# Kernel optimization log

Hardware: AMD Instinct MI355X
Metric: run time of the kernel (lower is better)

Reference implementation:

```python
import jax, jax.numpy as jnp
import numpy as np

N = 50000      # nodes
E = 1_600_000  # edges per metapath graph
M = 3          # meta-path patterns
D = 128        # feature dim (in_size == out_size, GraphConv has no weight)
H = 128        # semantic-attention hidden size


def setup_inputs() -> dict:
    key = jax.random.key(0)
    k1, k2, k3, k4 = jax.random.split(key, 4)
    h = jax.random.normal(k1, (N, D), dtype=jnp.float32)
    # edges[m, 0] = src node ids, edges[m, 1] = dst node ids for metapath m
    edges = jax.random.randint(k2, (M, 2, E), 0, N, dtype=jnp.int32)
    W1 = jax.random.normal(k3, (D, H), dtype=jnp.float32) * 0.05
    b1 = jnp.zeros((H,), dtype=jnp.float32)
    W2 = jax.random.normal(k4, (H, 1), dtype=jnp.float32) * 0.05
    return {"h": h, "edges": edges, "W1": W1, "b1": b1, "W2": W2}


def _graph_conv_both(h, src, dst, n):
    """DGL GraphConv(norm='both', weight=None, bias=None):
    out = D_in^{-1/2} * A @ (D_out^{-1/2} * h), zero degrees clamped to 1."""
    ones = jnp.ones_like(src, dtype=h.dtype)
    out_deg = jax.ops.segment_sum(ones, src, num_segments=n)
    in_deg = jax.ops.segment_sum(ones, dst, num_segments=n)
    norm_src = jax.lax.rsqrt(jnp.maximum(out_deg, 1.0))
    norm_dst = jax.lax.rsqrt(jnp.maximum(in_deg, 1.0))
    msg = (h * norm_src[:, None])[src]                  # [E, D] gather
    agg = jax.ops.segment_sum(msg, dst, num_segments=n)  # [N, D] scatter-add
    return agg * norm_dst[:, None]


def reference(h, edges, W1, b1, W2):
    n = h.shape[0]
    m = edges.shape[0]
    # One normalized sparse aggregation per meta-path (fixed small M).
    z = jnp.stack(
        [_graph_conv_both(h, edges[i, 0], edges[i, 1], n) for i in range(m)],
        axis=1,
    )  # [N, M, D]
    # Semantic attention: project -> tanh -> score, mean over nodes, softmax over M.
    w = jnp.mean(jnp.tanh(z @ W1 + b1) @ W2, axis=0)  # [M, 1]
    beta = jax.nn.softmax(w, axis=0)                  # [M, 1]
    return jnp.sum(beta[None, :, :] * z, axis=1)      # [N, D]
```

## Files before the change

kernel.cpp:

```cpp
#include <hip/hip_runtime.h>
#include <cstdint>
#include <cstddef>

typedef unsigned int  uint;
typedef unsigned short ushort;
typedef short bf16x8 __attribute__((ext_vector_type(8)));
typedef float f32x4  __attribute__((ext_vector_type(4)));

#define N_NODES 50000
#define N_EDGES 1600000
#define N_META  3
#define DIM     128

#define BKT       128
#define NBKT      391
#define BIN_CHUNK 4096
#define NCHUNK    391
#define CSR_CAP   5504
#define OCH       128
#define EPC       (N_EDGES / OCH)
#define OWORDS    12500
#define PREP_A    (N_META * OCH)
#define W1C_B     4

#define AT_TILE   64
#define AT_NBLK   782

__device__ __forceinline__ uint bf16rne(float f) {
    const uint u = __float_as_uint(f);
    return (u + 0x7FFFu + ((u >> 16) & 1u)) >> 16;
}
__device__ __forceinline__ float bflo(uint p) { return __uint_as_float(p << 16); }
__device__ __forceinline__ float bfhi(uint p) { return __uint_as_float(p & 0xFFFF0000u); }
__device__ __forceinline__ float fast_tanh(float x) {
    const float e = __expf(2.0f * x);
    return 1.0f - 2.0f / (e + 1.0f);
}

__global__ __launch_bounds__(256) void prep_kernel(
        const int* __restrict__ edges, const float* __restrict__ W1,
        int* __restrict__ bucket_cnt, uint* __restrict__ partials,
        ushort* __restrict__ W1T) {
    __shared__ __align__(16) uint sh[OWORDS];
    __shared__ uint bh[NBKT];
    const int blk = blockIdx.x;
    if (blk < PREP_A) {
        const int m = blk >> 7, c = blk & 127;
        uint4* sh4 = reinterpret_cast<uint4*>(sh);
        for (int j = threadIdx.x; j < OWORDS / 4; j += 256)
            sh4[j] = make_uint4(0u, 0u, 0u, 0u);
        for (int j = threadIdx.x; j < NBKT; j += 256) bh[j] = 0;
        __syncthreads();
        const int* src = edges + (size_t)(2 * m) * N_EDGES;
        const int* dst = edges + (size_t)(2 * m + 1) * N_EDGES;
        const int beg = c * EPC;
        for (int i = beg + 4 * threadIdx.x; i + 4 <= beg + EPC; i += 1024) {
            const uint4 s4 = *reinterpret_cast<const uint4*>(src + i);
            const uint4 d4 = *reinterpret_cast<const uint4*>(dst + i);
            atomicAdd(&sh[s4.x >> 2], 1u << (8 * (s4.x & 3)));
            atomicAdd(&sh[s4.y >> 2], 1u << (8 * (s4.y & 3)));
            atomicAdd(&sh[s4.z >> 2], 1u << (8 * (s4.z & 3)));
            atomicAdd(&sh[s4.w >> 2], 1u << (8 * (s4.w & 3)));
            atomicAdd(&bh[d4.x >> 7], 1u);
            atomicAdd(&bh[d4.y >> 7], 1u);
            atomicAdd(&bh[d4.z >> 7], 1u);
            atomicAdd(&bh[d4.w >> 7], 1u);
        }
        __syncthreads();
        uint4* outp4 = reinterpret_cast<uint4*>(
            partials + (size_t)(m * OCH + c) * OWORDS);
        for (int j = threadIdx.x; j < OWORDS / 4; j += 256) outp4[j] = sh4[j];
        for (int j = threadIdx.x; j < NBKT; j += 256)
            if (bh[j]) atomicAdd(&bucket_cnt[m * NBKT + j], (int)bh[j]);
    } else {
        const int base = (blk - PREP_A) * (DIM * DIM / W1C_B);
        for (int o = base + threadIdx.x; o < base + DIM * DIM / W1C_B; o += 256) {
            const int j = o >> 7, k = o & 127;
            W1T[o] = (ushort)bf16rne(W1[k * DIM + j]);
        }
    }
}

__global__ __launch_bounds__(512) void scan_nsrc_kernel(
        const int* __restrict__ bucket_cnt, int* __restrict__ bucket_off,
        int* __restrict__ bucket_cur, int* __restrict__ row_off,
        const uint* __restrict__ partials, float* __restrict__ nsrc) {
    const int blk = blockIdx.x;
    if (blk < N_META) {
        __shared__ int sc[512];
        const int m = blk, t = threadIdx.x;
        const int v = (t < NBKT) ? bucket_cnt[m * NBKT + t] : 0;
        sc[t] = v;
        __syncthreads();
        for (int off = 1; off < 512; off <<= 1) {
            const int tt = (t >= off) ? sc[t - off] : 0;
            __syncthreads();
            sc[t] += tt;
            __syncthreads();
        }
        const int excl = sc[t] - v;
        if (t < NBKT) {
            bucket_off[m * (NBKT + 1) + t] = excl;
            bucket_cur[m * NBKT + t] = excl;
        }
        if (t == 0) {
            bucket_off[m * (NBKT + 1) + NBKT] = N_EDGES;
            row_off[m * (N_NODES + 1) + N_NODES] = N_EDGES;
        }
    } else {
        const int i = (blk - N_META) * 512 + threadIdx.x;
        if (i < N_META * N_NODES) {
            const int m = i / N_NODES, node = i - m * N_NODES;
            const int q = node >> 2, s8 = 8 * (node & 3);
            int s = 0;
#pragma unroll 8
            for (int c = 0; c < OCH; ++c)
                s += (partials[(size_t)(m * OCH + c) * OWORDS + q] >> s8) & 0xFF;
            nsrc[i] = rsqrtf(fmaxf((float)s, 1.0f));
        }
    }
}

__global__ __launch_bounds__(256) void scale_kernel(
        const float* __restrict__ h, const float* __restrict__ nsrc,
        ushort* __restrict__ hbm) {
    const int i = blockIdx.x * 256 + threadIdx.x;
    const int node = i >> 5;
    const float4 v = reinterpret_cast<const float4*>(h)[i];
    uint2* o = reinterpret_cast<uint2*>(hbm);
#pragma unroll
    for (int m = 0; m < N_META; ++m) {
        const float n = nsrc[m * N_NODES + node];
        uint2 p;
        p.x = bf16rne(v.x * n) | (bf16rne(v.y * n) << 16);
        p.y = bf16rne(v.z * n) | (bf16rne(v.w * n) << 16);
        o[(size_t)m * (N_NODES * DIM / 4) + i] = p;
    }
}

__global__ __launch_bounds__(256) void bin_kernel(
        const int* __restrict__ edges, int* __restrict__ bucket_cur,
        uint* __restrict__ pairs) {
    const int m = blockIdx.y;
    __shared__ int hist[NBKT];
    __shared__ int cur[NBKT];
    for (int j = threadIdx.x; j < NBKT; j += 256) hist[j] = 0;
    __syncthreads();
    const int* src = edges + (size_t)(2 * m) * N_EDGES;
    const int* dst = edges + (size_t)(2 * m + 1) * N_EDGES;
    const int beg = blockIdx.x * BIN_CHUNK;
    const int end = min(beg + BIN_CHUNK, N_EDGES);
    for (int i = beg + 4 * threadIdx.x; i + 4 <= end; i += 1024) {
        const uint4 d4 = *reinterpret_cast<const uint4*>(dst + i);
        atomicAdd(&hist[d4.x >> 7], 1);
        atomicAdd(&hist[d4.y >> 7], 1);
        atomicAdd(&hist[d4.z >> 7], 1);
        atomicAdd(&hist[d4.w >> 7], 1);
    }
    __syncthreads();
    for (int j = threadIdx.x; j < NBKT; j += 256) {
        const int n = hist[j];
        cur[j] = n ? atomicAdd(&bucket_cur[m * NBKT + j], n) : 0;
    }
    __syncthreads();
    uint* pm = pairs + (size_t)m * N_EDGES;
    for (int i = beg + 4 * threadIdx.x; i + 4 <= end; i += 1024) {
        const uint4 s4 = *reinterpret_cast<const uint4*>(src + i);
        const uint4 d4 = *reinterpret_cast<const uint4*>(dst + i);
        int p0 = atomicAdd(&cur[d4.x >> 7], 1);
        pm[p0] = (d4.x << 16) | s4.x;
        int p1 = atomicAdd(&cur[d4.y >> 7], 1);
        pm[p1] = (d4.y << 16) | s4.y;
        int p2 = atomicAdd(&cur[d4.z >> 7], 1);
        pm[p2] = (d4.z << 16) | s4.z;
        int p3 = atomicAdd(&cur[d4.w >> 7], 1);
        pm[p3] = (d4.w << 16) | s4.w;
    }
}

__global__ __launch_bounds__(128) void csr_kernel(
        const uint* __restrict__ pairs, const int* __restrict__ bucket_off,
        int* __restrict__ row_off, ushort* __restrict__ csr) {
    const int b = blockIdx.x, m = blockIdx.y;
    const int node_base = b * BKT;
    const int nb = min(BKT, N_NODES - node_base);
    __shared__ uint stage[CSR_CAP];
    __shared__ int hist[BKT];
    __shared__ int sc[BKT];
    __shared__ int cur[BKT];
    hist[threadIdx.x] = 0;
    __syncthreads();
    const int beg = bucket_off[m * (NBKT + 1) + b];
    const int end = bucket_off[m * (NBKT + 1) + b + 1];
    const int cnt = end - beg;
    const uint* pm = pairs + (size_t)m * N_EDGES + beg;
    for (int i = threadIdx.x; i < cnt; i += 128) {
        const uint p = pm[i];
        if (i < CSR_CAP) stage[i] = p;
        atomicAdd(&hist[(int)(p >> 16) - node_base], 1);
    }
    __syncthreads();
    const int v = hist[threadIdx.x];
    sc[threadIdx.x] = v;
    __syncthreads();
    for (int off = 1; off < BKT; off <<= 1) {
        const int t = (threadIdx.x >= off) ? sc[threadIdx.x - off] : 0;
        __syncthreads();
        sc[threadIdx.x] += t;
        __syncthreads();
    }
    const int excl = sc[threadIdx.x] - v;
    cur[threadIdx.x] = beg + excl;
    if (threadIdx.x < nb)
        row_off[m * (N_NODES + 1) + node_base + threadIdx.x] = beg + excl;
    __syncthreads();
    ushort* cm = csr + (size_t)m * N_EDGES;
    for (int i = threadIdx.x; i < cnt; i += 128) {
        const uint p = (i < CSR_CAP) ? stage[i] : pm[i];
        const int dl = (int)(p >> 16) - node_base;
        const int pos = atomicAdd(&cur[dl], 1);
        cm[pos] = (ushort)(p & 0xFFFFu);
    }
}

__global__ __launch_bounds__(256) void gather_kernel(
        const ushort* __restrict__ hbm, const ushort* __restrict__ csr,
        const int* __restrict__ row_off, ushort* __restrict__ zb) {
    const int m    = blockIdx.y;
    const int wave = threadIdx.x >> 6;
    const int lane = threadIdx.x & 63;
    const int q    = lane >> 4;
    const int c16  = lane & 15;
    const int node = blockIdx.x * 4 + wave;
    const int* ro = row_off + m * (N_NODES + 1);
    const int beg = ro[node];
    const int end = ro[node + 1];
    const ushort* srcs = csr + (size_t)m * N_EDGES;
    const ushort* tab  = hbm + (size_t)m * N_NODES * DIM;
    float acc[8] = {};
    int j = beg;
    for (; j + 16 <= end; j += 16) {
        int s[4]; uint4 hv[4];
#pragma unroll
        for (int u = 0; u < 4; ++u) s[u] = srcs[j + 4 * u + q];
#pragma unroll
        for (int u = 0; u < 4; ++u)
            hv[u] = *reinterpret_cast<const uint4*>(tab + (size_t)s[u] * DIM + c16 * 8);
#pragma unroll
        for (int u = 0; u < 4; ++u) {
            acc[0] += bflo(hv[u].x); acc[1] += bfhi(hv[u].x);
            acc[2] += bflo(hv[u].y); acc[3] += bfhi(hv[u].y);
            acc[4] += bflo(hv[u].z); acc[5] += bfhi(hv[u].z);
            acc[6] += bflo(hv[u].w); acc[7] += bfhi(hv[u].w);
        }
    }
    for (; j + 4 <= end; j += 4) {
        const int s0 = srcs[j + q];
        const uint4 hv = *reinterpret_cast<const uint4*>(tab + (size_t)s0 * DIM + c16 * 8);
        acc[0] += bflo(hv.x); acc[1] += bfhi(hv.x);
        acc[2] += bflo(hv.y); acc[3] += bfhi(hv.y);
        acc[4] += bflo(hv.z); acc[5] += bfhi(hv.z);
        acc[6] += bflo(hv.w); acc[7] += bfhi(hv.w);
    }
    if (j + q < end) {
        const int s0 = srcs[j + q];
        const uint4 hv = *reinterpret_cast<const uint4*>(tab + (size_t)s0 * DIM + c16 * 8);
        acc[0] += bflo(hv.x); acc[1] += bfhi(hv.x);
        acc[2] += bflo(hv.y); acc[3] += bfhi(hv.y);
        acc[4] += bflo(hv.z); acc[5] += bfhi(hv.z);
        acc[6] += bflo(hv.w); acc[7] += bfhi(hv.w);
    }
#pragma unroll
    for (int k = 0; k < 8; ++k) {
        acc[k] += __shfl_xor(acc[k], 16);
        acc[k] += __shfl_xor(acc[k], 32);
    }
    if (lane < 16) {
        const float nd = rsqrtf(fmaxf((float)(end - beg), 1.0f));
        uint4 o;
        o.x = bf16rne(acc[0] * nd) | (bf16rne(acc[1] * nd) << 16);
        o.y = bf16rne(acc[2] * nd) | (bf16rne(acc[3] * nd) << 16);
        o.z = bf16rne(acc[4] * nd) | (bf16rne(acc[5] * nd) << 16);
        o.w = bf16rne(acc[6] * nd) | (bf16rne(acc[7] * nd) << 16);
        *reinterpret_cast<uint4*>(
            zb + ((size_t)m * N_NODES + node) * DIM + c16 * 8) = o;
    }
}

__global__ __launch_bounds__(256) void attn_kernel(
        const ushort* __restrict__ zb, const ushort* __restrict__ W1T,
        const float* __restrict__ b1, const float* __restrict__ W2,
        float* __restrict__ wacc) {
    const int m   = blockIdx.y;
    const int tid = threadIdx.x;
    const int wv  = tid >> 6;
    const int l   = tid & 63;
    __shared__ __align__(16) ushort w1s[DIM * DIM];
    __shared__ float red[4];

    {
        const uint4* g = reinterpret_cast<const uint4*>(W1T);
        for (int i = tid; i < DIM * DIM / 8; i += 256) {
            const int j = i >> 4;
            const int slot = i ^ (j & 7);
            *reinterpret_cast<uint4*>(
                reinterpret_cast<char*>(w1s) + slot * 16) = g[i];
        }
    }
    __syncthreads();

    const int node_base = blockIdx.x * AT_TILE + wv * 16;
    const int row = l & 15;
    const int q   = l >> 4;
    int nload = node_base + row;
    if (nload >= N_NODES) nload = N_NODES - 1;
    const ushort* zrow = zb + ((size_t)m * N_NODES + nload) * DIM + q * 8;

    bf16x8 a[4];
#pragma unroll
    for (int kk = 0; kk < 4; ++kk)
        a[kk] = *reinterpret_cast<const bf16x8*>(zrow + kk * 32);

    f32x4 acc[8];
#pragma unroll
    for (int ct = 0; ct < 8; ++ct) acc[ct] = (f32x4){0.f, 0.f, 0.f, 0.f};

#pragma unroll
    for (int kk = 0; kk < 4; ++kk) {
#pragma unroll
        for (int ct = 0; ct < 8; ++ct) {
            const int j = ct * 16 + row;
            const int slot = (j * 16 + kk * 4 + q) ^ (j & 7);
            const bf16x8 b = *reinterpret_cast<const bf16x8*>(
                reinterpret_cast<char*>(w1s) + slot * 16);
            acc[ct] = __builtin_amdgcn_mfma_f32_16x16x32_bf16(
                a[kk], b, acc[ct], 0, 0, 0);
        }
    }

    float local = 0.0f;
#pragma unroll
    for (int ct = 0; ct < 8; ++ct) {
        const int j = ct * 16 + row;
        const float b1j = b1[j];
        const float w2j = W2[j];
#pragma unroll
        for (int r = 0; r < 4; ++r) {
            const int nd = node_base + q * 4 + r;
            if (nd < N_NODES)
                local += fast_tanh(acc[ct][r] + b1j) * w2j;
        }
    }
    for (int off = 32; off > 0; off >>= 1)
        local += __shfl_xor(local, off);
    if (l == 0) red[wv] = local;
    __syncthreads();
    if (tid == 0)
        atomicAdd(&wacc[m], red[0] + red[1] + red[2] + red[3]);
}

__global__ __launch_bounds__(256) void final_kernel(
        const ushort* __restrict__ zb, const float* __restrict__ wacc,
        float* __restrict__ out) {
    const int g = blockIdx.x * 256 + threadIdx.x;
    const float invN = 1.0f / (float)N_NODES;
    const float w0 = wacc[0] * invN, w1 = wacc[1] * invN, w2 = wacc[2] * invN;
    const float mx = fmaxf(w0, fmaxf(w1, w2));
    const float e0 = expf(w0 - mx), e1 = expf(w1 - mx), e2 = expf(w2 - mx);
    const float inv = 1.0f / (e0 + e1 + e2);
    const float beta[3] = {e0 * inv, e1 * inv, e2 * inv};
    float a[8] = {};
#pragma unroll
    for (int m = 0; m < N_META; ++m) {
        const uint4 v = reinterpret_cast<const uint4*>(zb)[
            (size_t)m * (N_NODES * DIM / 8) + g];
        const float bm = beta[m];
        a[0] = fmaf(bflo(v.x), bm, a[0]); a[1] = fmaf(bfhi(v.x), bm, a[1]);
        a[2] = fmaf(bflo(v.y), bm, a[2]); a[3] = fmaf(bfhi(v.y), bm, a[3]);
        a[4] = fmaf(bflo(v.z), bm, a[4]); a[5] = fmaf(bfhi(v.z), bm, a[5]);
        a[6] = fmaf(bflo(v.w), bm, a[6]); a[7] = fmaf(bfhi(v.w), bm, a[7]);
    }
    float4 o0 = {a[0], a[1], a[2], a[3]};
    float4 o1 = {a[4], a[5], a[6], a[7]};
    reinterpret_cast<float4*>(out)[(size_t)g * 2 + 0] = o0;
    reinterpret_cast<float4*>(out)[(size_t)g * 2 + 1] = o1;
}

extern "C" void kernel_launch(void* const* d_in, const int* in_sizes, int n_in,
                              void* d_out, int out_size, void* d_ws, size_t ws_size,
                              hipStream_t stream) {
    const float* h    = (const float*)d_in[0];
    const int*  edges = (const int*)d_in[1];
    const float* W1   = (const float*)d_in[2];
    const float* b1   = (const float*)d_in[3];
    const float* W2   = (const float*)d_in[4];
    float* out = (float*)d_out;

    char* p = (char*)d_ws;
    ushort* zb      = (ushort*)p;
    uint*  pairs    = (uint*)p;
    uint*  partials = (uint*)(p + (size_t)N_META * N_EDGES * 4);
    p += (size_t)N_META * N_NODES * DIM * 2;
    ushort* hbm     = (ushort*)p; p += (size_t)N_META * N_NODES * DIM * 2;
    ushort* csr     = (ushort*)p; p += (size_t)N_META * N_EDGES * 2;
    int* row_off    = (int*)p;    p += ((size_t)N_META * (N_NODES + 1) + 1) * 4;
    float* nsrc     = (float*)p;  p += (size_t)N_META * N_NODES * 4;
    float* wacc     = (float*)p;  p += 16 * 4;
    int* bucket_cnt = (int*)p;    p += (size_t)N_META * NBKT * 4;
    int* bucket_off = (int*)p;    p += (size_t)N_META * (NBKT + 1) * 4 + 4;
    int* bucket_cur = (int*)p;    p += (size_t)N_META * NBKT * 4;
    ushort* W1T     = (ushort*)p; p += (size_t)DIM * DIM * 2;

    hipMemsetAsync(wacc, 0, (16 + (size_t)N_META * NBKT) * 4, stream);

    prep_kernel<<<dim3(PREP_A + W1C_B), 256, 0, stream>>>(
        edges, W1, bucket_cnt, partials, W1T);
    scan_nsrc_kernel<<<dim3(N_META + (N_META * N_NODES + 511) / 512), 512, 0, stream>>>(
        bucket_cnt, bucket_off, bucket_cur, row_off, partials, nsrc);
    scale_kernel<<<dim3(N_NODES * DIM / 4 / 256), 256, 0, stream>>>(h, nsrc, hbm);
    bin_kernel<<<dim3(NCHUNK, N_META), 256, 0, stream>>>(edges, bucket_cur, pairs);
    csr_kernel<<<dim3(NBKT, N_META), 128, 0, stream>>>(pairs, bucket_off, row_off, csr);
    gather_kernel<<<dim3(N_NODES / 4, N_META), 256, 0, stream>>>(
        hbm, csr, row_off, zb);
    attn_kernel<<<dim3(AT_NBLK, N_META), 256, 0, stream>>>(zb, W1T, b1, W2, wacc);
    final_kernel<<<dim3(N_NODES * DIM / 8 / 256), 256, 0, stream>>>(zb, wacc, out);
}
```

Baseline: 389.8 us.

## Drop per-metapath scaled bf16 tables; apply source norm during gather

Removes scale_kernel, which wrote three source-norm-scaled bf16 copies of h, and replaces it with one unscaled bf16 copy of h built inside prep_kernel by extra blocks. The gather kernel now loads the per-source norm scalar alongside each row and applies it with fma. This cuts a launch and shrinks the gathered table from three copies to one, which should give better cache reuse across metapaths. The cost is an extra scattered scalar load per edge in the gather, plus slightly different rounding because the scaling now happens after the bf16 conversion.

```diff
diff --git a/kernel.cpp b/kernel.cpp
--- a/kernel.cpp
+++ b/kernel.cpp
@@ -22,6 +22,7 @@
 #define OWORDS    12500
 #define PREP_A    (N_META * OCH)
 #define W1C_B     4
+#define CONV_B    64
 
 #define AT_TILE   64
 #define AT_NBLK   782
@@ -39,8 +40,9 @@
 
 __global__ __launch_bounds__(256) void prep_kernel(
         const int* __restrict__ edges, const float* __restrict__ W1,
-        int* __restrict__ bucket_cnt, uint* __restrict__ partials,
-        ushort* __restrict__ W1T) {
+        const float* __restrict__ h, int* __restrict__ bucket_cnt,
+        uint* __restrict__ partials, ushort* __restrict__ W1T,
+        ushort* __restrict__ hb) {
     __shared__ __align__(16) uint sh[OWORDS];
     __shared__ uint bh[NBKT];
     const int blk = blockIdx.x;
@@ -72,11 +74,21 @@
         for (int j = threadIdx.x; j < OWORDS / 4; j += 256) outp4[j] = sh4[j];
         for (int j = threadIdx.x; j < NBKT; j += 256)
             if (bh[j]) atomicAdd(&bucket_cnt[m * NBKT + j], (int)bh[j]);
-    } else {
+    } else if (blk < PREP_A + W1C_B) {
         const int base = (blk - PREP_A) * (DIM * DIM / W1C_B);
         for (int o = base + threadIdx.x; o < base + DIM * DIM / W1C_B; o += 256) {
             const int j = o >> 7, k = o & 127;
             W1T[o] = (ushort)bf16rne(W1[k * DIM + j]);
+        }
+    } else {
+        const int b = blk - PREP_A - W1C_B;
+        const int total = N_NODES * DIM / 4;
+        for (int i = b * 256 + threadIdx.x; i < total; i += CONV_B * 256) {
+            const float4 v = reinterpret_cast<const float4*>(h)[i];
+            uint2 o;
+            o.x = bf16rne(v.x) | (bf16rne(v.y) << 16);
+            o.y = bf16rne(v.z) | (bf16rne(v.w) << 16);
+            reinterpret_cast<uint2*>(hb)[i] = o;
         }
     }
 }
@@ -121,23 +133,6 @@
     }
 }
 
-__global__ __launch_bounds__(256) void scale_kernel(
-        const float* __restrict__ h, const float* __restrict__ nsrc,
-        ushort* __restrict__ hbm) {
-    const int i = blockIdx.x * 256 + threadIdx.x;
-    const int node = i >> 5;
-    const float4 v = reinterpret_cast<const float4*>(h)[i];
-    uint2* o = reinterpret_cast<uint2*>(hbm);
-#pragma unroll
-    for (int m = 0; m < N_META; ++m) {
-        const float n = nsrc[m * N_NODES + node];
-        uint2 p;
-        p.x = bf16rne(v.x * n) | (bf16rne(v.y * n) << 16);
-        p.y = bf16rne(v.z * n) | (bf16rne(v.w * n) << 16);
-        o[(size_t)m * (N_NODES * DIM / 4) + i] = p;
-    }
-}
-
 __global__ __launch_bounds__(256) void bin_kernel(
         const int* __restrict__ edges, int* __restrict__ bucket_cur,
         uint* __restrict__ pairs) {
@@ -224,8 +219,9 @@
 }
 
 __global__ __launch_bounds__(256) void gather_kernel(
-        const ushort* __restrict__ hbm, const ushort* __restrict__ csr,
-        const int* __restrict__ row_off, ushort* __restrict__ zb) {
+        const ushort* __restrict__ hb, const ushort* __restrict__ csr,
+        const int* __restrict__ row_off, const float* __restrict__ nsrc,
+        ushort* __restrict__ zb) {
     const int m    = blockIdx.y;
     const int wave = threadIdx.x >> 6;
     const int lane = threadIdx.x & 63;
@@ -236,39 +232,55 @@
     const int beg = ro[node];
     const int end = ro[node + 1];
     const ushort* srcs = csr + (size_t)m * N_EDGES;
-    const ushort* tab  = hbm + (size_t)m * N_NODES * DIM;
+    const float* ns = nsrc + m * N_NODES;
     float acc[8] = {};
     int j = beg;
     for (; j + 16 <= end; j += 16) {
-        int s[4]; uint4 hv[4];
+        int s[4]; float n[4]; uint4 hv[4];
 #pragma unroll
         for (int u = 0; u < 4; ++u) s[u] = srcs[j + 4 * u + q];
 #pragma unroll
-        for (int u = 0; u < 4; ++u)
-            hv[u] = *reinterpret_cast<const uint4*>(tab + (size_t)s[u] * DIM + c16 * 8);
-#pragma unroll
         for (int u = 0; u < 4; ++u) {
-            acc[0] += bflo(hv[u].x); acc[1] += bfhi(hv[u].x);
-            acc[2] += bflo(hv[u].y); acc[3] += bfhi(hv[u].y);
-            acc[4] += bflo(hv[u].z); acc[5] += bfhi(hv[u].z);
-            acc[6] += bflo(hv[u].w); acc[7] += bfhi(hv[u].w);
+            n[u]  = ns[s[u]];
+            hv[u] = *reinterpret_cast<const uint4*>(hb + (size_t)s[u] * DIM + c16 * 8);
+        }
+#pragma unroll
+        for (int u = 0; u < 4; ++u) {
+            acc[0] = fmaf(bflo(hv[u].x), n[u], acc[0]);
+            acc[1] = fmaf(bfhi(hv[u].x), n[u], acc[1]);
+            acc[2] = fmaf(bflo(hv[u].y), n[u], acc[2]);
+            acc[3] = fmaf(bfhi(hv[u].y), n[u], acc[3]);
+            acc[4] = fmaf(bflo(hv[u].z), n[u], acc[4]);
+            acc[5] = fmaf(bfhi(hv[u].z), n[u], acc[5]);
+            acc[6] = fmaf(bflo(hv[u].w), n[u], acc[6]);
+            acc[7] = fmaf(bfhi(hv[u].w), n[u], acc[7]);
         }
     }
     for (; j + 4 <= end; j += 4) {
         const int s0 = srcs[j + q];
-        const uint4 hv = *reinterpret_cast<const uint4*>(tab + (size_t)s0 * DIM + c16 * 8);
-        acc[0] += bflo(hv.x); acc[1] += bfhi(hv.x);
-        acc[2] += bflo(hv.y); acc[3] += bfhi(hv.y);
-        acc[4] += bflo(hv.z); acc[5] += bfhi(hv.z);
-        acc[6] += bflo(hv.w); acc[7] += bfhi(hv.w);
+        const float n0 = ns[s0];
+        const uint4 hv = *reinterpret_cast<const uint4*>(hb + (size_t)s0 * DIM + c16 * 8);
+        acc[0] = fmaf(bflo(hv.x), n0, acc[0]);
+        acc[1] = fmaf(bfhi(hv.x), n0, acc[1]);
+        acc[2] = fmaf(bflo(hv.y), n0, acc[2]);
+        acc[3] = fmaf(bfhi(hv.y), n0, acc[3]);
+        acc[4] = fmaf(bflo(hv.z), n0, acc[4]);
+        acc[5] = fmaf(bfhi(hv.z), n0, acc[5]);
+        acc[6] = fmaf(bflo(hv.w), n0, acc[6]);
+        acc[7] = fmaf(bfhi(hv.w), n0, acc[7]);
     }
     if (j + q < end) {
         const int s0 = srcs[j + q];
-        const uint4 hv = *reinterpret_cast<const uint4*>(tab + (size_t)s0 * DIM + c16 * 8);
-        acc[0] += bflo(hv.x); acc[1] += bfhi(hv.x);
-        acc[2] += bflo(hv.y); acc[3] += bfhi(hv.y);
-        acc[4] += bflo(hv.z); acc[5] += bfhi(hv.z);
-        acc[6] += bflo(hv.w); acc[7] += bfhi(hv.w);
+        const float n0 = ns[s0];
+        const uint4 hv = *reinterpret_cast<const uint4*>(hb + (size_t)s0 * DIM + c16 * 8);
+        acc[0] = fmaf(bflo(hv.x), n0, acc[0]);
+        acc[1] = fmaf(bfhi(hv.x), n0, acc[1]);
+        acc[2] = fmaf(bflo(hv.y), n0, acc[2]);
+        acc[3] = fmaf(bfhi(hv.y), n0, acc[3]);
+        acc[4] = fmaf(bflo(hv.z), n0, acc[4]);
+        acc[5] = fmaf(bfhi(hv.z), n0, acc[5]);
+        acc[6] = fmaf(bflo(hv.w), n0, acc[6]);
+        acc[7] = fmaf(bfhi(hv.w), n0, acc[7]);
     }
 #pragma unroll
     for (int k = 0; k < 8; ++k) {
@@ -401,7 +413,7 @@
     uint*  pairs    = (uint*)p;
     uint*  partials = (uint*)(p + (size_t)N_META * N_EDGES * 4);
     p += (size_t)N_META * N_NODES * DIM * 2;
-    ushort* hbm     = (ushort*)p; p += (size_t)N_META * N_NODES * DIM * 2;
+    ushort* hb      = (ushort*)p; p += (size_t)N_NODES * DIM * 2;
     ushort* csr     = (ushort*)p; p += (size_t)N_META * N_EDGES * 2;
     int* row_off    = (int*)p;    p += ((size_t)N_META * (N_NODES + 1) + 1) * 4;
     float* nsrc     = (float*)p;  p += (size_t)N_META * N_NODES * 4;
@@ -413,15 +425,14 @@
 
     hipMemsetAsync(wacc, 0, (16 + (size_t)N_META * NBKT) * 4, stream);
 
-    prep_kernel<<<dim3(PREP_A + W1C_B), 256, 0, stream>>>(
-        edges, W1, bucket_cnt, partials, W1T);
+    prep_kernel<<<dim3(PREP_A + W1C_B + CONV_B), 256, 0, stream>>>(
+        edges, W1, h, bucket_cnt, partials, W1T, hb);
     scan_nsrc_kernel<<<dim3(N_META + (N_META * N_NODES + 511) / 512), 512, 0, stream>>>(
         bucket_cnt, bucket_off, bucket_cur, row_off, partials, nsrc);
-    scale_kernel<<<dim3(N_NODES * DIM / 4 / 256), 256, 0, stream>>>(h, nsrc, hbm);
     bin_kernel<<<dim3(NCHUNK, N_META), 256, 0, stream>>>(edges, bucket_cur, pairs);
     csr_kernel<<<dim3(NBKT, N_META), 128, 0, stream>>>(pairs, bucket_off, row_off, csr);
     gather_kernel<<<dim3(N_NODES / 4, N_META), 256, 0, stream>>>(
-        hbm, csr, row_off, zb);
+        hb, csr, row_off, nsrc, zb);
     attn_kernel<<<dim3(AT_NBLK, N_META), 256, 0, stream>>>(zb, W1T, b1, W2, wacc);
     final_kernel<<<dim3(N_NODES * DIM / 8 / 256), 256, 0, stream>>>(zb, wacc, out);
 }
```

Result: no change. 396.9 us (+1.8%).
